# Kernel optimization log

Hardware: AMD Instinct MI355X
Metric: run time of the kernel (lower is better)

## Reference

```python
import jax, jax.numpy as jnp
import numpy as np

B, T, S, H = 8, 256, 256, 512

def setup_inputs() -> dict:
    key = jax.random.key(0)
    k1, k2, k3, k4, k5, k6 = jax.random.split(key, 6)
    query = jax.random.normal(k1, (B, T, H), dtype=jnp.float32)
    encoder_outputs = jax.random.normal(k2, (B, S, H), dtype=jnp.float32)
    # lengths in [1, S] so every row has at least one valid source position
    src_lengths = jax.random.randint(k3, (B,), 1, S + 1, dtype=jnp.int64)
    scale = 1.0 / np.sqrt(H)
    W_h = jax.random.normal(k4, (H, H), dtype=jnp.float32) * scale  # nn.Linear weight (out, in)
    W_s = jax.random.normal(k5, (H, H), dtype=jnp.float32) * scale
    v = jax.random.normal(k6, (H,), dtype=jnp.float32) * scale     # nn.Linear(H,1) weight squeezed
    return {"query": query, "encoder_outputs": encoder_outputs,
            "src_lengths": src_lengths, "W_h": W_h, "W_s": W_s, "v": v}

def reference(query, encoder_outputs, src_lengths, W_h, W_s, v):
    # Linear without bias: y = x @ W^T
    enc_f = jnp.einsum('bsh,oh->bso', encoder_outputs, W_h)   # (B,S,H)
    qry_f = jnp.einsum('bth,oh->bto', query, W_s)             # (B,T,H)
    # additive score: v^T tanh(enc_f + qry_f), broadcast over (T,S)
    scores = jnp.einsum('btsh,h->bts',
                        jnp.tanh(enc_f[:, None, :, :] + qry_f[:, :, None, :]), v)  # (B,T,S)
    mask = jnp.arange(S)[None, :] >= src_lengths[:, None]      # (B,S) True = pad
    scores = jnp.where(mask[:, None, :], -jnp.inf, scores)
    attn_weights = jax.nn.softmax(scores, axis=-1)             # (B,T,S)
    attn_out = jnp.einsum('bts,bsh->bth', attn_weights, encoder_outputs)
    return attn_out
```

## Files before the change

kernel.cpp:

```cpp
#include <hip/hip_runtime.h>
#include <cstddef>
#include <math.h>

#define BD 8
#define TD 256
#define SD 256
#define HD 512
#define K2F 2.885390081777927f

#define EXP2(x) __builtin_amdgcn_exp2f(x)
#define RCP(x)  __builtin_amdgcn_rcpf(x)

typedef __attribute__((ext_vector_type(8))) _Float16 half8;
typedef __attribute__((ext_vector_type(4))) _Float16 half4;
typedef __attribute__((ext_vector_type(4))) float float4v;

__device__ __forceinline__ float exp2_sat(float x) {
    return EXP2(fminf(fmaxf(x, -80.0f), 80.0f));
}

#define LSTR 40

__global__ __launch_bounds__(1024) void projK(
    const float* __restrict__ enc, const float* __restrict__ qry,
    const float* __restrict__ Wh,  const float* __restrict__ Ws,
    float* __restrict__ encT, float* __restrict__ encS, float* __restrict__ qryf)
{
    __shared__ float smem[2560];

    const int bid = blockIdx.x;
    const int tid = threadIdx.x;
    const int l  = tid & 63;
    const int w  = tid >> 6;
    const int rf = l & 15;
    const int q  = l >> 4;

    _Float16* LA = (_Float16*)smem;
    _Float16* LB = (_Float16*)(smem + 1280);

    const int x  = bid & 7;
    const int k  = bid >> 3;
    const bool isq = k >= 32;
    const int kk = k & 31;
    const int my = (isq ? 32 : 0) + x * 4 + (kk & 3);
    const int n0 = (kk >> 2) * 64;
    const int m0 = my * 64;

    const bool stagesA = (tid < 512);
    const int srow = (tid >> 3) & 63;
    const int scol = (tid & 7) * 4;
    const float* Sbase = stagesA
        ? (isq ? qry + (size_t)(m0 - 2048 + srow) * HD
               : enc + (size_t)(m0 + srow) * HD) + scol
        : (isq ? Ws : Wh) + (size_t)(n0 + srow) * HD + scol;
    _Float16* Ldst = (stagesA ? LA : LB) + srow * LSTR + scol;

    const int mi = (w & 3) * 16;
    const int ni = (w >> 2) * 16;

    float4v acc = {0, 0, 0, 0};

    float4 a0 = *(const float4*)(Sbase);

    for (int ks = 0; ks < 16; ++ks) {
        if (ks) __syncthreads();
        {
            half4 ha;
            ha[0]=(_Float16)a0.x; ha[1]=(_Float16)a0.y; ha[2]=(_Float16)a0.z; ha[3]=(_Float16)a0.w;
            *(half4*)Ldst = ha;
        }
        __syncthreads();
        if (ks + 1 < 16) a0 = *(const float4*)(Sbase + (ks + 1) * 32);
        half8 ah = *(const half8*)&LA[(mi + rf) * LSTR + q * 8];
        half8 bh = *(const half8*)&LB[(ni + rf) * LSTR + q * 8];
        acc = __builtin_amdgcn_mfma_f32_16x16x32_f16(ah, bh, acc, 0, 0, 0);
    }

    if (!isq) {
        const int b  = m0 >> 8;
        const int sb = (m0 & 255) + mi + q * 4;
        const int h  = n0 + ni + rf;
        float e0 = exp2_sat(acc[0]*K2F), e1 = exp2_sat(acc[1]*K2F);
        float e2 = exp2_sat(acc[2]*K2F), e3 = exp2_sat(acc[3]*K2F);
        *(float4*)(encT + (size_t)b * HD * SD + (size_t)h * SD + sb) =
            make_float4(e0, e1, e2, e3);
        float* es = encS + ((size_t)b * SD + sb) * HD + h;
        es[0 * HD] = e0; es[1 * HD] = e1; es[2 * HD] = e2; es[3 * HD] = e3;
    } else {
        const int mrow = (m0 - 2048) + mi + q * 4;
        #pragma unroll
        for (int r = 0; r < 4; ++r)
            qryf[(size_t)(mrow + r) * HD + n0 + ni + rf] = exp2_sat(acc[r] * K2F);
    }
}

__global__ __launch_bounds__(1024) void scoreS(
    const float* __restrict__ encS, const float* __restrict__ qryf,
    const float* __restrict__ v, const int* __restrict__ lens,
    float* __restrict__ part2)
{
    __shared__ float qls[4096];

    const int bid = blockIdx.x;
    const int tid = threadIdx.x;
    const int b      = bid & 7;
    const int rest   = bid >> 3;
    const int toct   = rest & 31;
    const int schunk = rest >> 5;
    const int t0     = toct * 8;
    const int len    = lens[b];

    if (schunk * 16 >= len) return;

    {
        const float* qf = qryf + ((size_t)b * TD + t0) * HD;
        const int i = tid * 4;
        *(float4*)&qls[i] = *(const float4*)(qf + (i >> 9) * HD + (i & 511));
    }
    __syncthreads();

    const int l = tid & 63;
    const int w = tid >> 6;
    const int s = schunk * 16 + w;

    if (s < len) {
        const float* eb = encS + ((size_t)b * SD + s) * HD;
        float a[8];
        #pragma unroll
        for (int t = 0; t < 8; ++t) a[t] = 0.0f;

        #pragma unroll
        for (int i = 0; i < 2; ++i) {
            const int j0 = i * 256 + 4 * l;
            float4 e4 = *(const float4*)(eb + j0);
            float4 v4 = *(const float4*)(v + j0);
            #pragma unroll
            for (int t = 0; t < 8; ++t) {
                float4 q4 = *(const float4*)&qls[t * 512 + j0];
                float p;
                p = fmaf(e4.x, q4.x, 1.0f); a[t] = fmaf(v4.x, RCP(p), a[t]);
                p = fmaf(e4.y, q4.y, 1.0f); a[t] = fmaf(v4.y, RCP(p), a[t]);
                p = fmaf(e4.z, q4.z, 1.0f); a[t] = fmaf(v4.z, RCP(p), a[t]);
                p = fmaf(e4.w, q4.w, 1.0f); a[t] = fmaf(v4.w, RCP(p), a[t]);
            }
        }

        float my = 0.0f;
        #pragma unroll
        for (int t = 0; t < 8; ++t) {
            float x = a[t];
            #pragma unroll
            for (int off = 32; off; off >>= 1) x += __shfl_xor(x, off);
            if (l == t) my = x;
        }
        if (l < 8)
            part2[((size_t)b * TD + t0 + l) * SD + s] = my;
    }
}

__global__ __launch_bounds__(512) void attn3K(
    const float* __restrict__ enc, const float* __restrict__ part2,
    const int* __restrict__ lens, float* __restrict__ out)
{
    __shared__ float avred[8192];
    __shared__ float wls[4 * SD];

    const int bid = blockIdx.x;
    const int tid = threadIdx.x;
    const int b   = bid & 7;
    const int t0  = (bid >> 3) * 4;
    const int w   = tid >> 6;
    const int l   = tid & 63;

    if (w < 4) {
        const int t = w;
        const int s0 = l * 4;
        float4 h0 = *(const float4*)(part2 + ((size_t)b * TD + t0 + t) * SD + s0);
        float p[4] = {h0.x, h0.y, h0.z, h0.w};
        const int len = lens[b];
        float sc[4];
        #pragma unroll
        for (int c = 0; c < 4; ++c)
            sc[c] = (s0 + c < len) ? -2.0f * p[c] : -INFINITY;
        float mx = fmaxf(fmaxf(sc[0], sc[1]), fmaxf(sc[2], sc[3]));
        #pragma unroll
        for (int off = 32; off; off >>= 1) mx = fmaxf(mx, __shfl_xor(mx, off));
        float ex[4]; float sum = 0.0f;
        #pragma unroll
        for (int c = 0; c < 4; ++c) { ex[c] = __expf(sc[c] - mx); sum += ex[c]; }
        #pragma unroll
        for (int off = 32; off; off >>= 1) sum += __shfl_xor(sum, off);
        const float inv = RCP(sum);
        *(float4*)&wls[t * SD + s0] = make_float4(ex[0]*inv, ex[1]*inv, ex[2]*inv, ex[3]*inv);
    }
    __syncthreads();

    const int g  = tid >> 7;
    const int h4 = (tid & 127) * 4;
    {
        const float* eb = enc + (size_t)b * SD * HD + h4;
        float4 o[4] = {{0,0,0,0},{0,0,0,0},{0,0,0,0},{0,0,0,0}};
        #pragma unroll 2
        for (int ss = 0; ss < 64; ++ss) {
            const int s = g * 64 + ss;
            float4 evv = *(const float4*)(eb + (size_t)s * HD);
            float wt[4];
            #pragma unroll
            for (int t = 0; t < 4; ++t) wt[t] = wls[t * SD + s];
            #pragma unroll
            for (int t = 0; t < 4; ++t) {
                o[t].x = fmaf(wt[t], evv.x, o[t].x);
                o[t].y = fmaf(wt[t], evv.y, o[t].y);
                o[t].z = fmaf(wt[t], evv.z, o[t].z);
                o[t].w = fmaf(wt[t], evv.w, o[t].w);
            }
        }
        #pragma unroll
        for (int t = 0; t < 4; ++t)
            *(float4*)&avred[(size_t)(g * 4 + t) * 512 + h4] = o[t];
    }
    __syncthreads();
    {
        const int t  = tid >> 7;
        const int hh = (tid & 127) * 4;
        float4 r = {0, 0, 0, 0};
        #pragma unroll
        for (int gg = 0; gg < 4; ++gg) {
            float4 x = *(const float4*)&avred[(size_t)(gg * 4 + t) * 512 + hh];
            r.x += x.x; r.y += x.y; r.z += x.z; r.w += x.w;
        }
        *(float4*)(out + ((size_t)b * TD + t0 + t) * HD + hh) = r;
    }
}

__global__ __launch_bounds__(1024) void attnK(
    const float* __restrict__ enc, const float* __restrict__ encT,
    const float* __restrict__ qryf, const float* __restrict__ v,
    const int* __restrict__ lens, float* __restrict__ out)
{
    __shared__ float smem[14336];

    const int bid = blockIdx.x;
    const int tid = threadIdx.x;
    const int b   = bid & 7;
    const int t0  = (bid >> 3) * 8;
    const int l = tid & 63;
    const int w = tid >> 6;

    float* qls = smem;
    float* pls = smem + 4096;
    float* wls = smem + 12288;

    {
        const float* qf = qryf + ((size_t)b * TD + t0) * HD;
        const int j = tid & 511;
        #pragma unroll
        for (int t = (tid >> 9); t < 8; t += 2)
            qls[t * 512 + j] = qf[t * HD + j];
    }
    __syncthreads();

    float a[8][4];
    #pragma unroll
    for (int t = 0; t < 8; ++t)
        #pragma unroll
        for (int c = 0; c < 4; ++c) a[t][c] = 0.0f;
    {
        const int jbase = w * 32;
        const float* ep = encT + (size_t)b * HD * SD + (size_t)jbase * SD + l * 4;
        #pragma unroll 4
        for (int jj = 0; jj < 32; ++jj) {
            float4 e = *(const float4*)(ep + (size_t)jj * SD);
            float vj = v[jbase + jj];
            float qv[8];
            #pragma unroll
            for (int t = 0; t < 8; ++t) qv[t] = qls[t * 512 + jbase + jj];
            float ev[4] = {e.x, e.y, e.z, e.w};
            #pragma unroll
            for (int t = 0; t < 8; ++t)
                #pragma unroll
                for (int c = 0; c < 4; ++c) {
                    float p = fmaf(ev[c], qv[t], 1.0f);
                    a[t][c] = fmaf(vj, RCP(p), a[t][c]);
                }
        }
    }
    if (w < 4) {
        #pragma unroll
        for (int t = 0; t < 8; ++t)
            *(float4*)&pls[(w * 8 + t) * 256 + l * 4] =
                make_float4(a[t][0], a[t][1], a[t][2], a[t][3]);
    }
    __syncthreads();
    if (w >= 4 && w < 8) {
        #pragma unroll
        for (int t = 0; t < 8; ++t) {
            float4 c4 = *(const float4*)&pls[((w - 4) * 8 + t) * 256 + l * 4];
            c4.x += a[t][0]; c4.y += a[t][1]; c4.z += a[t][2]; c4.w += a[t][3];
            *(float4*)&pls[((w - 4) * 8 + t) * 256 + l * 4] = c4;
        }
    }
    __syncthreads();
    if (w >= 8 && w < 12) {
        #pragma unroll
        for (int t = 0; t < 8; ++t) {
            float4 c4 = *(const float4*)&pls[((w - 8) * 8 + t) * 256 + l * 4];
            c4.x += a[t][0]; c4.y += a[t][1]; c4.z += a[t][2]; c4.w += a[t][3];
            *(float4*)&pls[((w - 8) * 8 + t) * 256 + l * 4] = c4;
        }
    }
    __syncthreads();
    if (w >= 12) {
        #pragma unroll
        for (int t = 0; t < 8; ++t) {
            float4 c4 = *(const float4*)&pls[((w - 12) * 8 + t) * 256 + l * 4];
            c4.x += a[t][0]; c4.y += a[t][1]; c4.z += a[t][2]; c4.w += a[t][3];
            *(float4*)&pls[((w - 12) * 8 + t) * 256 + l * 4] = c4;
        }
    }
    __syncthreads();

    if (w < 8) {
        const int t = w;
        float p[4] = {0, 0, 0, 0};
        #pragma unroll
        for (int g = 0; g < 4; ++g) {
            float4 pp = *(const float4*)&pls[(g * 8 + t) * 256 + l * 4];
            p[0] += pp.x; p[1] += pp.y; p[2] += pp.z; p[3] += pp.w;
        }
        const int len = lens[b];
        const int s0 = l * 4;
        float sc[4];
        #pragma unroll
        for (int c = 0; c < 4; ++c)
            sc[c] = (s0 + c < len) ? -2.0f * p[c] : -INFINITY;
        float mx = fmaxf(fmaxf(sc[0], sc[1]), fmaxf(sc[2], sc[3]));
        #pragma unroll
        for (int off = 32; off; off >>= 1) mx = fmaxf(mx, __shfl_xor(mx, off));
        float ex[4]; float sum = 0.0f;
        #pragma unroll
        for (int c = 0; c < 4; ++c) { ex[c] = __expf(sc[c] - mx); sum += ex[c]; }
        #pragma unroll
        for (int off = 32; off; off >>= 1) sum += __shfl_xor(sum, off);
        const float inv = RCP(sum);
        *(float4*)&wls[t * SD + s0] = make_float4(ex[0]*inv, ex[1]*inv, ex[2]*inv, ex[3]*inv);
    }
    __syncthreads();

    const int sg = tid >> 7;
    const int h4 = (tid & 127) * 4;
    float* avred = pls;
    float4 o[8];
    #pragma unroll
    for (int t = 0; t < 8; ++t) o[t] = make_float4(0.f, 0.f, 0.f, 0.f);
    {
        const float* eb = enc + (size_t)b * SD * HD + h4;
        #pragma unroll 2
        for (int ss = 0; ss < 32; ++ss) {
            const int s = sg * 32 + ss;
            float4 evv = *(const float4*)(eb + (size_t)s * HD);
            float wt[8];
            #pragma unroll
            for (int t = 0; t < 8; ++t) wt[t] = wls[t * SD + s];
            #pragma unroll
            for (int t = 0; t < 8; ++t) {
                o[t].x = fmaf(wt[t], evv.x, o[t].x);
                o[t].y = fmaf(wt[t], evv.y, o[t].y);
                o[t].z = fmaf(wt[t], evv.z, o[t].z);
                o[t].w = fmaf(wt[t], evv.w, o[t].w);
            }
        }
    }
    if (sg < 2) {
        #pragma unroll
        for (int t = 0; t < 8; ++t)
            *(float4*)&avred[(size_t)(sg * 8 + t) * 512 + h4] = o[t];
    }
    __syncthreads();
    if (sg >= 2 && sg < 4) {
        #pragma unroll
        for (int t = 0; t < 8; ++t) {
            float4 c4 = *(const float4*)&avred[(size_t)((sg - 2) * 8 + t) * 512 + h4];
            c4.x += o[t].x; c4.y += o[t].y; c4.z += o[t].z; c4.w += o[t].w;
            *(float4*)&avred[(size_t)((sg - 2) * 8 + t) * 512 + h4] = c4;
        }
    }
    __syncthreads();
    if (sg >= 4 && sg < 6) {
        #pragma unroll
        for (int t = 0; t < 8; ++t) {
            float4 c4 = *(const float4*)&avred[(size_t)((sg - 4) * 8 + t) * 512 + h4];
            c4.x += o[t].x; c4.y += o[t].y; c4.z += o[t].z; c4.w += o[t].w;
            *(float4*)&avred[(size_t)((sg - 4) * 8 + t) * 512 + h4] = c4;
        }
    }
    __syncthreads();
    if (sg >= 6) {
        #pragma unroll
        for (int t = 0; t < 8; ++t) {
            float4 c4 = *(const float4*)&avred[(size_t)((sg - 6) * 8 + t) * 512 + h4];
            c4.x += o[t].x; c4.y += o[t].y; c4.z += o[t].z; c4.w += o[t].w;
            *(float4*)&avred[(size_t)((sg - 6) * 8 + t) * 512 + h4] = c4;
        }
    }
    __syncthreads();

    {
        const int t  = tid >> 7;
        const int hh = (tid & 127) * 4;
        float4 x0 = *(const float4*)&avred[(size_t)(0 * 8 + t) * 512 + hh];
        float4 x1 = *(const float4*)&avred[(size_t)(1 * 8 + t) * 512 + hh];
        float4 r = make_float4(x0.x + x1.x, x0.y + x1.y, x0.z + x1.z, x0.w + x1.w);
        *(float4*)(out + ((size_t)b * TD + t0 + t) * HD + hh) = r;
    }
}

extern "C" void kernel_launch(void* const* d_in, const int* in_sizes, int n_in,
                              void* d_out, int out_size, void* d_ws, size_t ws_size,
                              hipStream_t stream) {
    const float* query = (const float*)d_in[0];
    const float* enc   = (const float*)d_in[1];
    const int*   lens  = (const int*)d_in[2];
    const float* W_h   = (const float*)d_in[3];
    const float* W_s   = (const float*)d_in[4];
    const float* v     = (const float*)d_in[5];
    float* out = (float*)d_out;

    char* ws = (char*)d_ws;
    float* encT  = (float*)(ws);
    float* qryf  = (float*)(ws + ((size_t)4 << 20));
    float* encS  = (float*)(ws + ((size_t)8 << 20));
    float* part2 = (float*)(ws + ((size_t)12 << 20));

    projK<<<dim3(512), dim3(1024), 0, stream>>>(enc, query, W_h, W_s, encT, encS, qryf);

    bool use_s = (ws_size >= ((size_t)14 << 20));
    hipFuncAttributes fa{};
    if (use_s &&
        hipFuncGetAttributes(&fa, (const void*)scoreS) == hipSuccess &&
        fa.localSizeBytes > 0) {
        use_s = false;
    }

    if (use_s) {
        scoreS<<<dim3(4096), dim3(1024), 0, stream>>>(encS, qryf, v, lens, part2);
        attn3K<<<dim3(512),  dim3(512),  0, stream>>>(enc, part2, lens, out);
    } else {
        attnK<<<dim3(256), dim3(1024), 0, stream>>>(enc, encT, qryf, v, lens, out);
    }
}
```

Measured before the change: 134.1 us.

## Make scoreS loop over source chunks with register-resident query and LDS reduction

scoreS now launches 512 blocks instead of 4096, and each block loops over eight 16-row source chunks. The query tile and v are loaded once into registers and reused for every chunk, which removes repeated LDS and global loads. The per-wave 8x6 shuffle reduction is replaced by a padded LDS transpose, a partial sum per lane, and three shuffles. In exchange, register pressure rises (64 floats of query are held in registers), and there is a risk of spilling, which would trigger the fallback path. Fewer blocks also means lower occupancy and less latency hiding.

```diff
diff --git a/kernel.cpp b/kernel.cpp
--- a/kernel.cpp
+++ b/kernel.cpp
@@ -94,23 +94,24 @@
     }
 }
 
-__global__ __launch_bounds__(1024) void scoreS(
+__global__ __launch_bounds__(1024, 1) void scoreS(
     const float* __restrict__ encS, const float* __restrict__ qryf,
     const float* __restrict__ v, const int* __restrict__ lens,
     float* __restrict__ part2)
 {
     __shared__ float qls[4096];
+    __shared__ float red[16 * 576];
 
     const int bid = blockIdx.x;
     const int tid = threadIdx.x;
-    const int b      = bid & 7;
-    const int rest   = bid >> 3;
-    const int toct   = rest & 31;
-    const int schunk = rest >> 5;
-    const int t0     = toct * 8;
-    const int len    = lens[b];
-
-    if (schunk * 16 >= len) return;
+    const int b    = bid >> 6;
+    const int rest = bid & 63;
+    const int toct = rest >> 1;
+    const int sh   = rest & 1;
+    const int t0   = toct * 8;
+    const int len  = lens[b];
+
+    if (sh * 128 >= len) return;
 
     {
         const float* qf = qryf + ((size_t)b * TD + t0) * HD;
@@ -121,9 +122,26 @@
 
     const int l = tid & 63;
     const int w = tid >> 6;
-    const int s = schunk * 16 + w;
-
-    if (s < len) {
+    float* rb = red + w * 576;
+
+    float4 qreg[2][8];
+    #pragma unroll
+    for (int i = 0; i < 2; ++i)
+        #pragma unroll
+        for (int t = 0; t < 8; ++t)
+            qreg[i][t] = *(const float4*)&qls[t * 512 + i * 256 + 4 * l];
+    float4 vreg[2];
+    #pragma unroll
+    for (int i = 0; i < 2; ++i)
+        vreg[i] = *(const float4*)(v + i * 256 + 4 * l);
+
+    const int tsel = l & 7;
+    const int ck   = l >> 3;
+
+    for (int k = 0; k < 8; ++k) {
+        const int s = sh * 128 + k * 16 + w;
+        if (s >= len) break;
+
         const float* eb = encS + ((size_t)b * SD + s) * HD;
         float a[8];
         #pragma unroll
@@ -131,12 +149,11 @@
 
         #pragma unroll
         for (int i = 0; i < 2; ++i) {
-            const int j0 = i * 256 + 4 * l;
-            float4 e4 = *(const float4*)(eb + j0);
-            float4 v4 = *(const float4*)(v + j0);
+            float4 e4 = *(const float4*)(eb + i * 256 + 4 * l);
+            float4 v4 = vreg[i];
             #pragma unroll
             for (int t = 0; t < 8; ++t) {
-                float4 q4 = *(const float4*)&qls[t * 512 + j0];
+                float4 q4 = qreg[i][t];
                 float p;
                 p = fmaf(e4.x, q4.x, 1.0f); a[t] = fmaf(v4.x, RCP(p), a[t]);
                 p = fmaf(e4.y, q4.y, 1.0f); a[t] = fmaf(v4.y, RCP(p), a[t]);
@@ -145,16 +162,17 @@
             }
         }
 
-        float my = 0.0f;
-        #pragma unroll
-        for (int t = 0; t < 8; ++t) {
-            float x = a[t];
-            #pragma unroll
-            for (int off = 32; off; off >>= 1) x += __shfl_xor(x, off);
-            if (l == t) my = x;
-        }
+        *(float4*)&rb[l * 9 + 0] = make_float4(a[0], a[1], a[2], a[3]);
+        *(float4*)&rb[l * 9 + 4] = make_float4(a[4], a[5], a[6], a[7]);
+        float part = 0.0f;
+        #pragma unroll
+        for (int i = 0; i < 8; ++i)
+            part += rb[(ck * 8 + i) * 9 + tsel];
+        part += __shfl_xor(part, 8);
+        part += __shfl_xor(part, 16);
+        part += __shfl_xor(part, 32);
         if (l < 8)
-            part2[((size_t)b * TD + t0 + l) * SD + s] = my;
+            part2[((size_t)b * TD + t0 + l) * SD + s] = part;
     }
 }
 
@@ -443,8 +461,8 @@
     }
 
     if (use_s) {
-        scoreS<<<dim3(4096), dim3(1024), 0, stream>>>(encS, qryf, v, lens, part2);
-        attn3K<<<dim3(512),  dim3(512),  0, stream>>>(enc, part2, lens, out);
+        scoreS<<<dim3(512), dim3(1024), 0, stream>>>(encS, qryf, v, lens, part2);
+        attn3K<<<dim3(512), dim3(512),  0, stream>>>(enc, part2, lens, out);
     } else {
         attnK<<<dim3(256), dim3(1024), 0, stream>>>(enc, encT, qryf, v, lens, out);
     }
```

Result: faster. 123.9 us (-7.6%).
